# Kernel tuning notes

Measured on AMD Instinct MI355X. Metric: run time of the kernel, lower is better.

Reference implementation:

```python
import jax, jax.numpy as jnp
import numpy as np


def _highway(x, Ws, bs):
    # Ws: [n_hw, 2H, H] (torch Linear layout), bs: [n_hw, 2H]
    H = x.shape[-1]
    for i in range(Ws.shape[0]):
        proj = jnp.einsum('bsh,oh->bso', x, Ws[i]) + bs[i]
        nonlin = jax.nn.relu(proj[..., :H])
        gate = jax.nn.sigmoid(proj[..., H:])
        x = gate * x + (1.0 - gate) * nonlin
    return x


def setup_inputs() -> dict:
    key = jax.random.key(0)
    ks = jax.random.split(key, 10)
    B, S, H, L, W, NHW = 32, 512, 512, 2, 4, 2
    scale = 1.0 / np.sqrt(H)
    return {
        'inputs': jax.random.normal(ks[0], (B, S, H), dtype=jnp.float32),
        'masks': jnp.ones((B, S), dtype=jnp.int32),
        'fwd_pads': jax.random.normal(ks[1], (L, W, H), dtype=jnp.float32) * scale,
        'bwd_pads': jax.random.normal(ks[2], (L, W, H), dtype=jnp.float32) * scale,
        'fwd_ws': jax.random.normal(ks[3], (L, W + 1), dtype=jnp.float32),
        'bwd_ws': jax.random.normal(ks[4], (L, W + 1), dtype=jnp.float32),
        'fwd_hw_W': jax.random.normal(ks[5], (L, NHW, 2 * H, H), dtype=jnp.float32) * scale,
        'fwd_hw_b': jax.random.normal(ks[6], (L, NHW, 2 * H), dtype=jnp.float32) * 0.1,
        'bwd_hw_W': jax.random.normal(ks[7], (L, NHW, 2 * H, H), dtype=jnp.float32) * scale,
        'bwd_hw_b': jax.random.normal(ks[8], (L, NHW, 2 * H), dtype=jnp.float32) * 0.1,
    }


def reference(inputs, masks, fwd_pads, bwd_pads, fwd_ws, bwd_ws,
              fwd_hw_W, fwd_hw_b, bwd_hw_W, bwd_hw_b):
    # inputs: [B,S,H]; masks unused (as in the torch module)
    B, S, H = inputs.shape
    L, W, _ = fwd_pads.shape
    fwd_in = inputs
    bwd_in = inputs
    outs = []
    for l in range(L):
        fp = jnp.broadcast_to(fwd_pads[l], (B, W, H))
        bp = jnp.broadcast_to(bwd_pads[l], (B, W, H))
        pf = jnp.concatenate([fp, fwd_in, bp], axis=1)  # [B, S+2W, H]
        pb = jnp.concatenate([fp, bwd_in, bp], axis=1)
        # forward window at t covers padded positions t..t+W (causal)
        f_win = jnp.stack([pf[:, k:k + S] for k in range(W + 1)], axis=0)  # [W+1,B,S,H]
        f_out = jnp.einsum('k,kbsh->bsh', fwd_ws[l], f_win)
        # backward window at t covers padded positions t+W..t+2W (anti-causal)
        b_win = jnp.stack([pb[:, W + k:W + k + S] for k in range(W + 1)], axis=0)
        b_out = jnp.einsum('k,kbsh->bsh', bwd_ws[l], b_win)
        f_out = _highway(f_out, fwd_hw_W[l], fwd_hw_b[l])
        b_out = _highway(b_out, bwd_hw_W[l], bwd_hw_b[l])
        fwd_in, bwd_in = f_out, b_out
        outs.append(jnp.concatenate([f_out, b_out], axis=-1))
    return jnp.stack(outs, axis=0)  # [L, B, S, 2H]
```

## Files before the change

kernel.cpp:

```cpp
#include <hip/hip_runtime.h>
#include <hip/hip_bf16.h>

typedef __attribute__((ext_vector_type(8))) short bf16x8;
typedef __attribute__((ext_vector_type(4))) float floatx4;

#define B_ 32
#define S_ 512
#define H_ 512
#define M_ (B_*S_)
#define K_ 512
#define N_ 1024

__device__ __forceinline__ void gload_lds16(const void* g, void* l) {
  __builtin_amdgcn_global_load_lds(
      (const __attribute__((address_space(1))) void*)g,
      (__attribute__((address_space(3))) void*)l, 16, 0, 0);
}

__global__ void cvt2_kernel(const float* __restrict__ s0, const float* __restrict__ s1,
                            __hip_bfloat16* __restrict__ d0, __hip_bfloat16* __restrict__ d1) {
  int t = blockIdx.x * 256 + threadIdx.x;
  const float* src;
  __hip_bfloat16* dst;
  int i;
  if (t < 524288) { src = s0; dst = d0; i = t; }
  else            { src = s1; dst = d1; i = t - 524288; }
  float4 v = *(const float4*)(src + (size_t)i * 4);
  union { ushort4 u; __hip_bfloat16 h[4]; } pk;
  pk.h[0] = __float2bfloat16(v.x);
  pk.h[1] = __float2bfloat16(v.y);
  pk.h[2] = __float2bfloat16(v.z);
  pk.h[3] = __float2bfloat16(v.w);
  *(ushort4*)((unsigned short*)dst + (size_t)i * 4) = pk.u;
}

__global__ void conv_kernel(const float* __restrict__ inf, const float* __restrict__ inb,
                            int instride,
                            const float* __restrict__ fpad, const float* __restrict__ bpad,
                            const float* __restrict__ fw, const float* __restrict__ bw,
                            __hip_bfloat16* __restrict__ xaf, __hip_bfloat16* __restrict__ xab) {
  int t = blockIdx.x * 256 + threadIdx.x;
  int dir = blockIdx.y;
  int row = t >> 7;
  int hv  = (t & 127) << 2;
  int s = row & (S_ - 1);
  float4 a = make_float4(0.f, 0.f, 0.f, 0.f);
  if (dir == 0) {
#pragma unroll
    for (int k = 0; k < 5; ++k) {
      float w = fw[k];
      const float* src = (s + k < 4) ? (fpad + (size_t)(s + k) * H_ + hv)
                                     : (inf + (size_t)(row + k - 4) * instride + hv);
      float4 v = *(const float4*)src;
      a.x += w * v.x; a.y += w * v.y; a.z += w * v.z; a.w += w * v.w;
    }
  } else {
#pragma unroll
    for (int k = 0; k < 5; ++k) {
      float w = bw[k];
      const float* src = (s + k < S_) ? (inb + (size_t)(row + k) * instride + hv)
                                      : (bpad + (size_t)(s + k - S_) * H_ + hv);
      float4 v = *(const float4*)src;
      a.x += w * v.x; a.y += w * v.y; a.z += w * v.z; a.w += w * v.w;
    }
  }
  __hip_bfloat16* xa = dir ? xab : xaf;
  union { ushort4 u; __hip_bfloat16 h[4]; } pk;
  pk.h[0] = __float2bfloat16(a.x);
  pk.h[1] = __float2bfloat16(a.y);
  pk.h[2] = __float2bfloat16(a.z);
  pk.h[3] = __float2bfloat16(a.w);
  *(ushort4*)((unsigned short*)xa + (size_t)row * H_ + hv) = pk.u;
}

__global__ __launch_bounds__(512, 4)
void hw_gemm(const __hip_bfloat16* __restrict__ Af, const __hip_bfloat16* __restrict__ Ab,
             const __hip_bfloat16* __restrict__ Wf, const __hip_bfloat16* __restrict__ Wb,
             const float* __restrict__ biasf, const float* __restrict__ biasb,
             __hip_bfloat16* __restrict__ Anf, __hip_bfloat16* __restrict__ Anb,
             float* __restrict__ outp, int final_mode) {
  __shared__ __align__(16) char smem[49152];

  const int tid = threadIdx.x;
  const int lane = tid & 63, wave = tid >> 6;
  const int wm = wave >> 2, wn = wave & 3;
  const int quad = lane >> 4, l16 = lane & 15;
  const int dir = blockIdx.z;

  const int n = blockIdx.x;
  const int mpanel = (n & 7) | ((n >> 5) << 3);
  const int bx = (n >> 3) & 3;
  const int m0 = mpanel * 128;
  const int h0 = bx * 128;

  const __hip_bfloat16* A = dir ? Ab : Af;
  const __hip_bfloat16* Wm = dir ? Wb : Wf;
  const float* bias = dir ? biasb : biasf;
  __hip_bfloat16* An = dir ? Anb : Anf;

  floatx4 acc[4][4];
#pragma unroll
  for (int i = 0; i < 4; ++i)
#pragma unroll
    for (int j = 0; j < 4; ++j) acc[i][j] = (floatx4){0.f, 0.f, 0.f, 0.f};

  const int srow = lane >> 2;
  const int skk  = (((lane & 3) ^ ((lane >> 3) & 3)) << 3);
  const int key  = (l16 >> 1) & 3;
  const int xkp  = bx * 4 + wn;

  const __hip_bfloat16* aptr = A + (size_t)(m0 + wave * 16 + srow) * K_ + skk;
  const __hip_bfloat16* bptr[2];
#pragma unroll
  for (int c = 0; c < 2; ++c) {
    const int brow = (wave * 2 + c) * 16 + srow;
    const int wnp = brow >> 6, rr = brow & 63;
    const int wrow = (rr < 32) ? (h0 + wnp * 32 + rr)
                               : (512 + h0 + wnp * 32 + (rr - 32));
    bptr[c] = Wm + (size_t)wrow * K_ + skk;
  }

  gload_lds16(aptr, smem + wave * 1024);
  gload_lds16(bptr[0], smem + 8192 + (wave * 2) * 1024);
  gload_lds16(bptr[1], smem + 8192 + (wave * 2 + 1) * 1024);
  __syncthreads();

  unsigned int xsp[4][2][2];
  int cur = 0;
  for (int kp = 0; kp < 16; ++kp) {
    const __hip_bfloat16* cA = (const __hip_bfloat16*)(smem + cur * 24576);
    const __hip_bfloat16* cB = (const __hip_bfloat16*)(smem + cur * 24576 + 8192);
    if (kp < 15) {
      char* nb = smem + (cur ^ 1) * 24576;
      const int kb = (kp + 1) * 32;
      gload_lds16(aptr + kb, nb + wave * 1024);
      gload_lds16(bptr[0] + kb, nb + 8192 + (wave * 2) * 1024);
      gload_lds16(bptr[1] + kb, nb + 8192 + (wave * 2 + 1) * 1024);
    }
    if (kp == xkp) {
      const unsigned short* pA = (const unsigned short*)cA;
#pragma unroll
      for (int i = 0; i < 4; ++i)
#pragma unroll
        for (int jj = 0; jj < 2; ++jj)
#pragma unroll
          for (int rh = 0; rh < 2; ++rh) {
            const int ra0 = wm * 64 + i * 16 + quad * 4 + rh * 2;
            const int ra1 = ra0 + 1;
            const int c2 = jj * 16 + l16;
            unsigned int lo = pA[ra0 * 32 + ((((c2 >> 3) ^ ((ra0 >> 1) & 3)) << 3) | (c2 & 7))];
            unsigned int hi = pA[ra1 * 32 + ((((c2 >> 3) ^ ((ra1 >> 1) & 3)) << 3) | (c2 & 7))];
            xsp[i][jj][rh] = lo | (hi << 16);
          }
    }
    bf16x8 av[4], bv[4];
#pragma unroll
    for (int i = 0; i < 4; ++i) {
      const int ra = wm * 64 + i * 16 + l16;
      av[i] = *(const bf16x8*)&cA[ra * 32 + ((quad ^ key) << 3)];
    }
#pragma unroll
    for (int j = 0; j < 4; ++j) {
      const int rb = wn * 64 + j * 16 + l16;
      bv[j] = *(const bf16x8*)&cB[rb * 32 + ((quad ^ key) << 3)];
    }
#pragma unroll
    for (int i = 0; i < 4; ++i)
#pragma unroll
      for (int j = 0; j < 4; ++j)
        acc[i][j] = __builtin_amdgcn_mfma_f32_16x16x32_bf16(av[i], bv[j], acc[i][j], 0, 0, 0);

    __syncthreads();
    cur ^= 1;
  }

  float bnl[2], bgt[2];
#pragma unroll
  for (int j = 0; j < 2; ++j) {
    const int c = h0 + wn * 32 + j * 16 + l16;
    bnl[j] = bias[c];
    bgt[j] = bias[512 + c];
  }

  if (final_mode) {
    float* ft = (float*)smem;
#pragma unroll
    for (int p = 0; p < 2; ++p) {
      if ((wn >> 1) == p) {
#pragma unroll
        for (int i = 0; i < 4; ++i)
#pragma unroll
          for (int r = 0; r < 4; ++r) {
            const int rl = wm * 64 + i * 16 + quad * 4 + r;
#pragma unroll
            for (int j = 0; j < 2; ++j) {
              float pn = acc[i][j][r] + bnl[j];
              float pg = acc[i][j + 2][r] + bgt[j];
              float g = 1.f / (1.f + __expf(-pg));
              unsigned int u = xsp[i][j][r >> 1];
              unsigned int bits = (r & 1) ? (u >> 16) : (u & 0xffffu);
              float xo = __uint_as_float(bits << 16);
              ft[rl * 64 + (wn & 1) * 32 + j * 16 + l16] =
                  g * xo + (1.f - g) * fmaxf(pn, 0.f);
            }
          }
      }
      __syncthreads();
#pragma unroll
      for (int q = 0; q < 4; ++q) {
        const int rl = q * 32 + (tid >> 4);
        const int cc = (tid & 15) * 4;
        float4 v = *(const float4*)&ft[rl * 64 + cc];
        *(float4*)&outp[(size_t)(m0 + rl) * N_ + dir * H_ + h0 + p * 64 + cc] = v;
      }
      __syncthreads();
    }
  } else {
    __hip_bfloat16* bt = (__hip_bfloat16*)smem;
#pragma unroll
    for (int i = 0; i < 4; ++i)
#pragma unroll
      for (int r = 0; r < 4; ++r) {
        const int rl = wm * 64 + i * 16 + quad * 4 + r;
#pragma unroll
        for (int j = 0; j < 2; ++j) {
          float pn = acc[i][j][r] + bnl[j];
          float pg = acc[i][j + 2][r] + bgt[j];
          float g = 1.f / (1.f + __expf(-pg));
          unsigned int u = xsp[i][j][r >> 1];
          unsigned int bits = (r & 1) ? (u >> 16) : (u & 0xffffu);
          float xo = __uint_as_float(bits << 16);
          bt[rl * 128 + wn * 32 + j * 16 + l16] =
              __float2bfloat16(g * xo + (1.f - g) * fmaxf(pn, 0.f));
        }
      }
    __syncthreads();
    const unsigned short* src = (const unsigned short*)smem;
#pragma unroll
    for (int p = 0; p < 4; ++p) {
      const int rl = p * 32 + (tid >> 4);
      const int cc = (tid & 15) * 8;
      int4 v = *(const int4*)(src + rl * 128 + cc);
      *(int4*)((unsigned short*)An + (size_t)(m0 + rl) * H_ + h0 + cc) = v;
    }
  }
}

extern "C" void kernel_launch(void* const* d_in, const int* in_sizes, int n_in,
                              void* d_out, int out_size, void* d_ws, size_t ws_size,
                              hipStream_t stream) {
  const float* inputs   = (const float*)d_in[0];
  const float* fwd_pads = (const float*)d_in[2];
  const float* bwd_pads = (const float*)d_in[3];
  const float* fwd_ws_p = (const float*)d_in[4];
  const float* bwd_ws_p = (const float*)d_in[5];
  const float* fwd_hw_W = (const float*)d_in[6];
  const float* fwd_hw_b = (const float*)d_in[7];
  const float* bwd_hw_W = (const float*)d_in[8];
  const float* bwd_hw_b = (const float*)d_in[9];
  float* out = (float*)d_out;

  char* ws = (char*)d_ws;
  size_t off = 0;
  __hip_bfloat16* Wbf = (__hip_bfloat16*)(ws + off); off += (size_t)4194304 * 2;
  __hip_bfloat16* xa0f = (__hip_bfloat16*)(ws + off); off += (size_t)M_ * H_ * 2;
  __hip_bfloat16* xa0b = (__hip_bfloat16*)(ws + off); off += (size_t)M_ * H_ * 2;
  __hip_bfloat16* xa1f = (__hip_bfloat16*)(ws + off); off += (size_t)M_ * H_ * 2;
  __hip_bfloat16* xa1b = (__hip_bfloat16*)(ws + off); off += (size_t)M_ * H_ * 2;

  cvt2_kernel<<<4096, 256, 0, stream>>>(fwd_hw_W, bwd_hw_W, Wbf, Wbf + (size_t)2097152);

  for (int l = 0; l < 2; ++l) {
    const float *inf, *inb;
    int instride;
    if (l == 0) { inf = inputs; inb = inputs; instride = H_; }
    else        { inf = out;    inb = out + H_; instride = N_; }
    conv_kernel<<<dim3(8192, 2), 256, 0, stream>>>(
        inf, inb, instride,
        fwd_pads + (size_t)l * 4 * H_, bwd_pads + (size_t)l * 4 * H_,
        fwd_ws_p + l * 5, bwd_ws_p + l * 5,
        xa0f, xa0b);

    hw_gemm<<<dim3(512, 1, 2), 512, 0, stream>>>(
        xa0f, xa0b,
        Wbf + (size_t)(l * 2) * 524288, Wbf + (size_t)2097152 + (size_t)(l * 2) * 524288,
        fwd_hw_b + (l * 2) * 1024, bwd_hw_b + (l * 2) * 1024,
        xa1f, xa1b, nullptr, 0);

    hw_gemm<<<dim3(512, 1, 2), 512, 0, stream>>>(
        xa1f, xa1b,
        Wbf + (size_t)(l * 2 + 1) * 524288, Wbf + (size_t)2097152 + (size_t)(l * 2 + 1) * 524288,
        fwd_hw_b + (l * 2 + 1) * 1024, bwd_hw_b + (l * 2 + 1) * 1024,
        nullptr, nullptr, out + (size_t)l * M_ * N_, 1);
  }
}
```

Baseline: 494.5 us.

## Keep the highway weight slice resident in LDS and stream activation tiles

The highway GEMM now loads a 64-column nonlin/gate weight slice (the full K) into LDS once per block using an XOR swizzle. It then streams two 256-row activation panels through a double-buffered LDS region. This is meant to cut repeated weight fetches and per-iteration B loads. In exchange it needs 160KB of dynamic LDS, which limits the CU to one block, and it doubles how often activations are re-read across column blocks. The weight preload is also not overlapped with compute.

```diff
diff --git a/kernel.cpp b/kernel.cpp
--- a/kernel.cpp
+++ b/kernel.cpp
@@ -73,106 +73,45 @@
   *(ushort4*)((unsigned short*)xa + (size_t)row * H_ + hv) = pk.u;
 }
 
-__global__ __launch_bounds__(512, 4)
+__global__ __launch_bounds__(512, 2)
 void hw_gemm(const __hip_bfloat16* __restrict__ Af, const __hip_bfloat16* __restrict__ Ab,
              const __hip_bfloat16* __restrict__ Wf, const __hip_bfloat16* __restrict__ Wb,
              const float* __restrict__ biasf, const float* __restrict__ biasb,
              __hip_bfloat16* __restrict__ Anf, __hip_bfloat16* __restrict__ Anb,
              float* __restrict__ outp, int final_mode) {
-  __shared__ __align__(16) char smem[49152];
+  extern __shared__ __align__(16) char smem[];
 
   const int tid = threadIdx.x;
   const int lane = tid & 63, wave = tid >> 6;
-  const int wm = wave >> 2, wn = wave & 3;
+  const int wm = wave >> 1, wn = wave & 1;
   const int quad = lane >> 4, l16 = lane & 15;
   const int dir = blockIdx.z;
 
   const int n = blockIdx.x;
-  const int mpanel = (n & 7) | ((n >> 5) << 3);
-  const int bx = (n >> 3) & 3;
-  const int m0 = mpanel * 128;
-  const int h0 = bx * 128;
+  const int by = n & 31, bx = n >> 5;
+  const int h0 = bx * 64;
 
   const __hip_bfloat16* A = dir ? Ab : Af;
   const __hip_bfloat16* Wm = dir ? Wb : Wf;
   const float* bias = dir ? biasb : biasf;
   __hip_bfloat16* An = dir ? Anb : Anf;
 
-  floatx4 acc[4][4];
-#pragma unroll
-  for (int i = 0; i < 4; ++i)
-#pragma unroll
-    for (int j = 0; j < 4; ++j) acc[i][j] = (floatx4){0.f, 0.f, 0.f, 0.f};
+  char* Abase = smem + 131072;
+
+#pragma unroll
+  for (int it = 0; it < 16; ++it) {
+    const int r = it * 8 + wave;
+    const int wn_ = r >> 6, rr = r & 63;
+    const int wrow = (rr < 32) ? (h0 + wn_ * 32 + rr)
+                               : (512 + h0 + wn_ * 32 + (rr - 32));
+    gload_lds16(Wm + (size_t)wrow * K_ + ((lane ^ wave) << 3),
+                smem + it * 8192 + wave * 1024);
+  }
 
   const int srow = lane >> 2;
   const int skk  = (((lane & 3) ^ ((lane >> 3) & 3)) << 3);
   const int key  = (l16 >> 1) & 3;
-  const int xkp  = bx * 4 + wn;
-
-  const __hip_bfloat16* aptr = A + (size_t)(m0 + wave * 16 + srow) * K_ + skk;
-  const __hip_bfloat16* bptr[2];
-#pragma unroll
-  for (int c = 0; c < 2; ++c) {
-    const int brow = (wave * 2 + c) * 16 + srow;
-    const int wnp = brow >> 6, rr = brow & 63;
-    const int wrow = (rr < 32) ? (h0 + wnp * 32 + rr)
-                               : (512 + h0 + wnp * 32 + (rr - 32));
-    bptr[c] = Wm + (size_t)wrow * K_ + skk;
-  }
-
-  gload_lds16(aptr, smem + wave * 1024);
-  gload_lds16(bptr[0], smem + 8192 + (wave * 2) * 1024);
-  gload_lds16(bptr[1], smem + 8192 + (wave * 2 + 1) * 1024);
-  __syncthreads();
-
-  unsigned int xsp[4][2][2];
-  int cur = 0;
-  for (int kp = 0; kp < 16; ++kp) {
-    const __hip_bfloat16* cA = (const __hip_bfloat16*)(smem + cur * 24576);
-    const __hip_bfloat16* cB = (const __hip_bfloat16*)(smem + cur * 24576 + 8192);
-    if (kp < 15) {
-      char* nb = smem + (cur ^ 1) * 24576;
-      const int kb = (kp + 1) * 32;
-      gload_lds16(aptr + kb, nb + wave * 1024);
-      gload_lds16(bptr[0] + kb, nb + 8192 + (wave * 2) * 1024);
-      gload_lds16(bptr[1] + kb, nb + 8192 + (wave * 2 + 1) * 1024);
-    }
-    if (kp == xkp) {
-      const unsigned short* pA = (const unsigned short*)cA;
-#pragma unroll
-      for (int i = 0; i < 4; ++i)
-#pragma unroll
-        for (int jj = 0; jj < 2; ++jj)
-#pragma unroll
-          for (int rh = 0; rh < 2; ++rh) {
-            const int ra0 = wm * 64 + i * 16 + quad * 4 + rh * 2;
-            const int ra1 = ra0 + 1;
-            const int c2 = jj * 16 + l16;
-            unsigned int lo = pA[ra0 * 32 + ((((c2 >> 3) ^ ((ra0 >> 1) & 3)) << 3) | (c2 & 7))];
-            unsigned int hi = pA[ra1 * 32 + ((((c2 >> 3) ^ ((ra1 >> 1) & 3)) << 3) | (c2 & 7))];
-            xsp[i][jj][rh] = lo | (hi << 16);
-          }
-    }
-    bf16x8 av[4], bv[4];
-#pragma unroll
-    for (int i = 0; i < 4; ++i) {
-      const int ra = wm * 64 + i * 16 + l16;
-      av[i] = *(const bf16x8*)&cA[ra * 32 + ((quad ^ key) << 3)];
-    }
-#pragma unroll
-    for (int j = 0; j < 4; ++j) {
-      const int rb = wn * 64 + j * 16 + l16;
-      bv[j] = *(const bf16x8*)&cB[rb * 32 + ((quad ^ key) << 3)];
-    }
-#pragma unroll
-    for (int i = 0; i < 4; ++i)
-#pragma unroll
-      for (int j = 0; j < 4; ++j)
-        acc[i][j] = __builtin_amdgcn_mfma_f32_16x16x32_bf16(av[i], bv[j], acc[i][j], 0, 0, 0);
-
-    __syncthreads();
-    cur ^= 1;
-  }
+  const int xkp  = bx * 2 + wn;
 
   float bnl[2], bgt[2];
 #pragma unroll
@@ -182,66 +121,139 @@
     bgt[j] = bias[512 + c];
   }
 
-  if (final_mode) {
-    float* ft = (float*)smem;
-#pragma unroll
-    for (int p = 0; p < 2; ++p) {
-      if ((wn >> 1) == p) {
+  const __hip_bfloat16* lW = (const __hip_bfloat16*)smem;
+
+  for (int half = 0; half < 2; ++half) {
+    const int m0 = by * 512 + half * 256;
+
+    const __hip_bfloat16* aptr[2];
+#pragma unroll
+    for (int c = 0; c < 2; ++c) {
+      const int chunk = wave * 2 + c;
+      aptr[c] = A + (size_t)(m0 + chunk * 16 + srow) * K_ + skk;
+    }
+
+    floatx4 acc[4][4];
+#pragma unroll
+    for (int i = 0; i < 4; ++i)
+#pragma unroll
+      for (int j = 0; j < 4; ++j) acc[i][j] = (floatx4){0.f, 0.f, 0.f, 0.f};
+
+#pragma unroll
+    for (int c = 0; c < 2; ++c)
+      gload_lds16(aptr[c], Abase + (wave * 2 + c) * 1024);
+    __syncthreads();
+
+    unsigned int xsp[4][2][2];
+    int cur = 0;
+    for (int kp = 0; kp < 16; ++kp) {
+      const __hip_bfloat16* cA = (const __hip_bfloat16*)(Abase + cur * 16384);
+      if (kp < 15) {
+        char* nb = Abase + (cur ^ 1) * 16384;
+        const int kb = (kp + 1) * 32;
+#pragma unroll
+        for (int c = 0; c < 2; ++c)
+          gload_lds16(aptr[c] + kb, nb + (wave * 2 + c) * 1024);
+      }
+      if (kp == xkp) {
+        const unsigned short* pA = (const unsigned short*)cA;
 #pragma unroll
         for (int i = 0; i < 4; ++i)
 #pragma unroll
-          for (int r = 0; r < 4; ++r) {
-            const int rl = wm * 64 + i * 16 + quad * 4 + r;
-#pragma unroll
-            for (int j = 0; j < 2; ++j) {
-              float pn = acc[i][j][r] + bnl[j];
-              float pg = acc[i][j + 2][r] + bgt[j];
-              float g = 1.f / (1.f + __expf(-pg));
-              unsigned int u = xsp[i][j][r >> 1];
-              unsigned int bits = (r & 1) ? (u >> 16) : (u & 0xffffu);
-              float xo = __uint_as_float(bits << 16);
-              ft[rl * 64 + (wn & 1) * 32 + j * 16 + l16] =
-                  g * xo + (1.f - g) * fmaxf(pn, 0.f);
+          for (int jj = 0; jj < 2; ++jj)
+#pragma unroll
+            for (int rh = 0; rh < 2; ++rh) {
+              const int ra0 = wm * 64 + i * 16 + quad * 4 + rh * 2;
+              const int ra1 = ra0 + 1;
+              const int c2 = jj * 16 + l16;
+              unsigned int lo = pA[ra0 * 32 + ((((c2 >> 3) ^ ((ra0 >> 1) & 3)) << 3) | (c2 & 7))];
+              unsigned int hi = pA[ra1 * 32 + ((((c2 >> 3) ^ ((ra1 >> 1) & 3)) << 3) | (c2 & 7))];
+              xsp[i][jj][rh] = lo | (hi << 16);
             }
+      }
+      bf16x8 av[4], bv[4];
+#pragma unroll
+      for (int i = 0; i < 4; ++i) {
+        const int ra = wm * 64 + i * 16 + l16;
+        av[i] = *(const bf16x8*)&cA[ra * 32 + ((quad ^ key) << 3)];
+      }
+#pragma unroll
+      for (int j = 0; j < 4; ++j) {
+        const int rb = wn * 64 + j * 16 + l16;
+        const int slot = (kp * 4 + quad) ^ (l16 & 7);
+        bv[j] = *(const bf16x8*)&lW[(size_t)rb * 512 + slot * 8];
+      }
+#pragma unroll
+      for (int i = 0; i < 4; ++i)
+#pragma unroll
+        for (int j = 0; j < 4; ++j)
+          acc[i][j] = __builtin_amdgcn_mfma_f32_16x16x32_bf16(av[i], bv[j], acc[i][j], 0, 0, 0);
+
+      __syncthreads();
+      cur ^= 1;
+    }
+
+    if (final_mode) {
+      float* ft = (float*)Abase;
+#pragma unroll
+      for (int p = 0; p < 2; ++p) {
+        if (wn == p) {
+#pragma unroll
+          for (int i = 0; i < 4; ++i)
+#pragma unroll
+            for (int r = 0; r < 4; ++r) {
+              const int rl = wm * 64 + i * 16 + quad * 4 + r;
+#pragma unroll
+              for (int j = 0; j < 2; ++j) {
+                float pn = acc[i][j][r] + bnl[j];
+                float pg = acc[i][j + 2][r] + bgt[j];
+                float g = 1.f / (1.f + __expf(-pg));
+                unsigned int u = xsp[i][j][r >> 1];
+                unsigned int bits = (r & 1) ? (u >> 16) : (u & 0xffffu);
+                float xo = __uint_as_float(bits << 16);
+                ft[rl * 32 + j * 16 + l16] = g * xo + (1.f - g) * fmaxf(pn, 0.f);
+              }
+            }
+        }
+        __syncthreads();
+#pragma unroll
+        for (int q = 0; q < 4; ++q) {
+          const int rl = q * 64 + (tid >> 3);
+          const int cc = (tid & 7) * 4;
+          float4 v = *(const float4*)&ft[rl * 32 + cc];
+          *(float4*)&outp[(size_t)(m0 + rl) * N_ + dir * H_ + h0 + p * 32 + cc] = v;
+        }
+        __syncthreads();
+      }
+    } else {
+      __hip_bfloat16* bt = (__hip_bfloat16*)Abase;
+#pragma unroll
+      for (int i = 0; i < 4; ++i)
+#pragma unroll
+        for (int r = 0; r < 4; ++r) {
+          const int rl = wm * 64 + i * 16 + quad * 4 + r;
+#pragma unroll
+          for (int j = 0; j < 2; ++j) {
+            float pn = acc[i][j][r] + bnl[j];
+            float pg = acc[i][j + 2][r] + bgt[j];
+            float g = 1.f / (1.f + __expf(-pg));
+            unsigned int u = xsp[i][j][r >> 1];
+            unsigned int bits = (r & 1) ? (u >> 16) : (u & 0xffffu);
+            float xo = __uint_as_float(bits << 16);
+            bt[rl * 64 + wn * 32 + j * 16 + l16] =
+                __float2bfloat16(g * xo + (1.f - g) * fmaxf(pn, 0.f));
           }
-      }
+        }
       __syncthreads();
-#pragma unroll
-      for (int q = 0; q < 4; ++q) {
-        const int rl = q * 32 + (tid >> 4);
-        const int cc = (tid & 15) * 4;
-        float4 v = *(const float4*)&ft[rl * 64 + cc];
-        *(float4*)&outp[(size_t)(m0 + rl) * N_ + dir * H_ + h0 + p * 64 + cc] = v;
+      const unsigned short* src = (const unsigned short*)Abase;
+#pragma unroll
+      for (int p = 0; p < 4; ++p) {
+        const int rl = p * 64 + (tid >> 3);
+        const int cc = (tid & 7) * 8;
+        int4 v = *(const int4*)(src + rl * 64 + cc);
+        *(int4*)((unsigned short*)An + (size_t)(m0 + rl) * H_ + h0 + cc) = v;
       }
       __syncthreads();
-    }
-  } else {
-    __hip_bfloat16* bt = (__hip_bfloat16*)smem;
-#pragma unroll
-    for (int i = 0; i < 4; ++i)
-#pragma unroll
-      for (int r = 0; r < 4; ++r) {
-        const int rl = wm * 64 + i * 16 + quad * 4 + r;
-#pragma unroll
-        for (int j = 0; j < 2; ++j) {
-          float pn = acc[i][j][r] + bnl[j];
-          float pg = acc[i][j + 2][r] + bgt[j];
-          float g = 1.f / (1.f + __expf(-pg));
-          unsigned int u = xsp[i][j][r >> 1];
-          unsigned int bits = (r & 1) ? (u >> 16) : (u & 0xffffu);
-          float xo = __uint_as_float(bits << 16);
-          bt[rl * 128 + wn * 32 + j * 16 + l16] =
-              __float2bfloat16(g * xo + (1.f - g) * fmaxf(pn, 0.f));
-        }
-      }
-    __syncthreads();
-    const unsigned short* src = (const unsigned short*)smem;
-#pragma unroll
-    for (int p = 0; p < 4; ++p) {
-      const int rl = p * 32 + (tid >> 4);
-      const int cc = (tid & 15) * 8;
-      int4 v = *(const int4*)(src + rl * 128 + cc);
-      *(int4*)((unsigned short*)An + (size_t)(m0 + rl) * H_ + h0 + cc) = v;
     }
   }
 }
@@ -260,6 +272,13 @@
   const float* bwd_hw_b = (const float*)d_in[9];
   float* out = (float*)d_out;
 
+  static int attr_done = 0;
+  if (!attr_done) {
+    (void)hipFuncSetAttribute((const void*)hw_gemm,
+                              hipFuncAttributeMaxDynamicSharedMemorySize, 163840);
+    attr_done = 1;
+  }
+
   char* ws = (char*)d_ws;
   size_t off = 0;
   __hip_bfloat16* Wbf = (__hip_bfloat16*)(ws + off); off += (size_t)4194304 * 2;
@@ -281,13 +300,13 @@
         fwd_ws_p + l * 5, bwd_ws_p + l * 5,
         xa0f, xa0b);
 
-    hw_gemm<<<dim3(512, 1, 2), 512, 0, stream>>>(
+    hw_gemm<<<dim3(256, 1, 2), 512, 163840, stream>>>(
         xa0f, xa0b,
         Wbf + (size_t)(l * 2) * 524288, Wbf + (size_t)2097152 + (size_t)(l * 2) * 524288,
         fwd_hw_b + (l * 2) * 1024, bwd_hw_b + (l * 2) * 1024,
         xa1f, xa1b, nullptr, 0);
 
-    hw_gemm<<<dim3(512, 1, 2), 512, 0, stream>>>(
+    hw_gemm<<<dim3(256, 1, 2), 512, 163840, stream>>>(
         xa1f, xa1b,
         Wbf + (size_t)(l * 2 + 1) * 524288, Wbf + (size_t)2097152 + (size_t)(l * 2 + 1) * 524288,
         fwd_hw_b + (l * 2 + 1) * 1024, bwd_hw_b + (l * 2 + 1) * 1024,
```

After: 449.9 us. -9.0%, faster.
